# Performance work log

Measured on AMD Instinct MI355X. Metric: run time of the kernel, lower is better.

The kernel has to match this reference:

```python
import jax, jax.numpy as jnp
import numpy as np

B, L, DM, H, PD = 2, 1024, 512, 8, 64
D = DM // H  # head_dim = 64
NEG = -10000.0


def setup_inputs() -> dict:
    key = jax.random.key(0)
    ks = jax.random.split(key, 12)
    s = 1.0 / np.sqrt(DM)
    sp = 1.0 / np.sqrt(PD)
    return {
        "x": jax.random.normal(ks[0], (B, L, DM), dtype=jnp.float32),
        "z": jax.random.normal(ks[1], (B, L, L, PD), dtype=jnp.float32),
        "residue_mask": jnp.ones((B, L), dtype=bool),
        "Wq": jax.random.normal(ks[2], (DM, DM), dtype=jnp.float32) * s,
        "bq": jnp.zeros((DM,), dtype=jnp.float32),
        "Wk": jax.random.normal(ks[3], (DM, DM), dtype=jnp.float32) * s,
        "bk": jnp.zeros((DM,), dtype=jnp.float32),
        "Wv": jax.random.normal(ks[4], (DM, DM), dtype=jnp.float32) * s,
        "bv": jnp.zeros((DM,), dtype=jnp.float32),
        "Wo": jax.random.normal(ks[5], (DM, DM), dtype=jnp.float32) * s,
        "bo": jnp.zeros((DM,), dtype=jnp.float32),
        "Wpb": jax.random.normal(ks[6], (PD, H), dtype=jnp.float32) * sp,
    }


def reference(x, z, residue_mask, Wq, bq, Wk, bk, Wv, bv, Wo, bo, Wpb):
    b, l, c = x.shape
    scale = 1.0 / np.sqrt(D)
    # projections -> (B, H, L, D)
    q = (x @ Wq + bq).reshape(b, l, H, D).transpose(0, 2, 1, 3)
    k = (x @ Wk + bk).reshape(b, l, H, D).transpose(0, 2, 1, 3)
    v = (x @ Wv + bv).reshape(b, l, H, D).transpose(0, 2, 1, 3)
    # pair bias: (B, L, L, PD) @ (PD, H) -> (B, H, L, L)
    bias = jnp.einsum('bijp,ph->bhij', z, Wpb)
    logits = jnp.einsum('bhid,bhjd->bhij', q, k) * scale + bias
    key_ok = residue_mask[:, None, None, :]
    query_ok = residue_mask[:, None, :, None]
    logits = jnp.where(key_ok, logits, NEG)
    logits = jnp.where(query_ok, logits, NEG)
    attn = jax.nn.softmax(logits, axis=-1)
    out = jnp.einsum('bhij,bhjd->bhid', attn, v)
    out = out.transpose(0, 2, 1, 3).reshape(b, l, c)
    return out @ Wo + bo
```

## Files before the change

### kernel.cpp

```cpp
#include <hip/hip_runtime.h>

typedef __bf16 bf16;
typedef __attribute__((ext_vector_type(4))) __bf16 bf16x4;
typedef __attribute__((ext_vector_type(8))) __bf16 bf16x8;
typedef __attribute__((ext_vector_type(4))) float f32x4;
typedef __attribute__((ext_vector_type(4))) _Float16 f16x4;
typedef __attribute__((ext_vector_type(2))) _Float16 f16x2;

#define B_   2
#define L_   1024
#define DM_  512
#define H_   8
#define D_   64
#define PD_  64
#define NEG_VAL -10000.0f

static __device__ __forceinline__ f32x4 mfma_bf16(bf16x8 a, bf16x8 b, f32x4 c) {
  return __builtin_amdgcn_mfma_f32_16x16x32_bf16(a, b, c, 0, 0, 0);
}

__global__ __launch_bounds__(256) void prep_bias(
    const float* __restrict__ z, const float* __restrict__ Wpb, const int* __restrict__ mask,
    const float* __restrict__ x, const float* __restrict__ Wq, const float* __restrict__ Wk,
    const float* __restrict__ Wv, const float* __restrict__ Wo,
    _Float16* __restrict__ biasbuf, bf16* __restrict__ xb, bf16* __restrict__ Wt,
    bf16* __restrict__ Wto) {
  __shared__ char smem[18944];
  int bid = blockIdx.x, tid = threadIdx.x;
  if (bid < 2048) {
    _Float16 (*outt)[1032] = (_Float16(*)[1032])smem;
    float* wpb_lds = (float*)(smem + 16512);
    int w = tid >> 6, lane = tid & 63;
    int lr = lane & 15, lg = lane >> 4;
    int jc = bid & 15, it = (bid >> 4) & 63, b = bid >> 10;
    if (tid < 128) {
      f32x4 v = reinterpret_cast<const f32x4*>(Wpb)[tid];
      *reinterpret_cast<f32x4*>(wpb_lds + tid * 4) = v;
    }
    __syncthreads();
    bf16x8 wb0, wb1;
#pragma unroll
    for (int e = 0; e < 8; ++e) {
      wb0[e] = (lr < 8) ? (bf16)wpb_lds[(lg * 8 + e) * 8 + lr] : (bf16)0.0f;
      wb1[e] = (lr < 8) ? (bf16)wpb_lds[(lg * 8 + 32 + e) * 8 + lr] : (bf16)0.0f;
    }
#pragma unroll
    for (int ii = 0; ii < 4; ++ii) {
      int il = w * 4 + ii;
      int i = it * 16 + il;
#pragma unroll
      for (int js = 0; js < 4; ++js) {
        const float* zr = z + ((long)(b * L_ + i) * L_ + jc * 64 + js * 16 + lr) * 64 + lg * 8;
        f32x4 z0 = *reinterpret_cast<const f32x4*>(zr);
        f32x4 z1 = *reinterpret_cast<const f32x4*>(zr + 4);
        f32x4 z2 = *reinterpret_cast<const f32x4*>(zr + 32);
        f32x4 z3 = *reinterpret_cast<const f32x4*>(zr + 36);
        bf16x8 a0, a1;
#pragma unroll
        for (int e = 0; e < 4; ++e) {
          a0[e] = (bf16)z0[e]; a0[e + 4] = (bf16)z1[e];
          a1[e] = (bf16)z2[e]; a1[e + 4] = (bf16)z3[e];
        }
        f32x4 c = {0.f, 0.f, 0.f, 0.f};
        c = mfma_bf16(a0, wb0, c);
        c = mfma_bf16(a1, wb1, c);
        if (lr < 8) {
          int4 mk = *reinterpret_cast<const int4*>(mask + b * L_ + jc * 64 + js * 16 + lg * 4);
          f16x4 hv;
          hv[0] = mk.x ? (_Float16)c[0] : (_Float16)NEG_VAL;
          hv[1] = mk.y ? (_Float16)c[1] : (_Float16)NEG_VAL;
          hv[2] = mk.z ? (_Float16)c[2] : (_Float16)NEG_VAL;
          hv[3] = mk.w ? (_Float16)c[3] : (_Float16)NEG_VAL;
          *reinterpret_cast<f16x4*>(&outt[lr][((js * 4 + lg) * 16 + il) * 4]) = hv;
        }
      }
    }
    __syncthreads();
    {
      int h = tid & 7, part = tid >> 3;
      _Float16* dst = biasbuf + (((((long)b * H_ + h) * 64 + it) * 16 + jc) << 10) + part * 32;
      const _Float16* srcl = &outt[h][part * 32];
#pragma unroll
      for (int e = 0; e < 8; ++e)
        *reinterpret_cast<f16x4*>(dst + e * 4) = *reinterpret_cast<const f16x4*>(srcl + e * 4);
    }
  } else {
    int pbid = bid - 2048;
    if (pbid < 1024) {
      float (*td)[33] = (float(*)[33])smem;
      int r = tid >> 3, c4 = (tid & 7) * 4;
      const float* src;
      bf16* dstbase;
      int n0, k0, srcol;
      if (pbid < 768) {
        int nt2 = pbid >> 4, kt = pbid & 15;
        n0 = nt2 * 32; k0 = kt * 32;
        int sel = n0 >> 9;
        src = sel == 0 ? Wq : (sel == 1 ? Wk : Wv);
        srcol = n0 & 511;
        dstbase = Wt + (long)n0 * 512;
      } else {
        int t2 = pbid - 768;
        int nt2 = t2 >> 4, kt = t2 & 15;
        n0 = nt2 * 32; k0 = kt * 32;
        src = Wo; srcol = n0;
        dstbase = Wto + (long)n0 * 512;
      }
      f32x4 v = *reinterpret_cast<const f32x4*>(src + (long)(k0 + r) * 512 + srcol + c4);
#pragma unroll
      for (int e = 0; e < 4; ++e) td[r][c4 + e] = v[e];
      __syncthreads();
      int nl = tid >> 3, k4 = (tid & 7) * 4;
      bf16x4 o;
#pragma unroll
      for (int e = 0; e < 4; ++e) o[e] = (bf16)td[k4 + e][nl];
      *reinterpret_cast<bf16x4*>(dstbase + (long)nl * 512 + k0 + k4) = o;
    } else {
      int base = (pbid - 1024) * 1024 + tid * 4;
      f32x4 v = *reinterpret_cast<const f32x4*>(x + base);
      bf16x4 o;
#pragma unroll
      for (int e = 0; e < 4; ++e) o[e] = (bf16)v[e];
      *reinterpret_cast<bf16x4*>(xb + base) = o;
    }
  }
}

__global__ __launch_bounds__(256) void qkv_gemm(
    const bf16* __restrict__ xb, const bf16* __restrict__ Wt,
    const float* __restrict__ bq, const float* __restrict__ bk, const float* __restrict__ bv,
    bf16* __restrict__ qb, bf16* __restrict__ kb, bf16* __restrict__ vT) {
  __shared__ bf16 bpanel[16 * 520];
  int tid = threadIdx.x, w = tid >> 6, lane = tid & 63;
  int lr = lane & 15, lg = lane >> 4;
  int bid = blockIdx.x;
  int mt = bid / 96, nt = bid - mt * 96;
  int col0 = nt * 16;
  {
    const bf16* src = Wt + (long)col0 * 512;
#pragma unroll
    for (int q = 0; q < 4; ++q) {
      int off = q * 2048 + tid * 8;
      int row = off >> 9, col = off & 511;
      *reinterpret_cast<bf16x8*>(&bpanel[row * 520 + col]) =
          *reinterpret_cast<const bf16x8*>(src + off);
    }
  }
  __syncthreads();
  int m0base = mt * 128 + w * 32;
  const bf16* a0p = xb + (long)(m0base + lr) * 512 + lg * 8;
  const bf16* a1p = a0p + 16 * 512;
  f32x4 acc0 = {0.f, 0.f, 0.f, 0.f}, acc1 = acc0;
#pragma unroll
  for (int kk = 0; kk < 512; kk += 32) {
    bf16x8 a0 = *reinterpret_cast<const bf16x8*>(a0p + kk);
    bf16x8 a1 = *reinterpret_cast<const bf16x8*>(a1p + kk);
    bf16x8 b = *reinterpret_cast<const bf16x8*>(&bpanel[lr * 520 + kk + lg * 8]);
    acc0 = mfma_bf16(a0, b, acc0);
    acc1 = mfma_bf16(a1, b, acc1);
  }
  int col = col0 + lr;
  int wsel = col >> 9;
  int ncol = col & 511;
  int h = ncol >> 6, d = ncol & 63;
  const float* bias = wsel == 0 ? bq : (wsel == 1 ? bk : bv);
  float bval = bias[ncol];
#pragma unroll
  for (int mi = 0; mi < 2; ++mi) {
    f32x4 acc = (mi == 0) ? acc0 : acc1;
    int m0 = m0base + mi * 16 + lg * 4;
    int bidx = m0 >> 10, l0 = m0 & 1023;
    if (wsel == 2) {
      bf16x4 pv;
#pragma unroll
      for (int r = 0; r < 4; ++r) pv[r] = (bf16)(acc[r] + bval);
      *reinterpret_cast<bf16x4*>(vT + ((long)(bidx * H_ + h) * D_ + d) * L_ + l0) = pv;
    } else if (wsel == 0) {
#pragma unroll
      for (int r = 0; r < 4; ++r)
        qb[((long)(bidx * H_ + h) * L_ + l0 + r) * D_ + d] = (bf16)((acc[r] + bval) * 0.125f);
    } else {
#pragma unroll
      for (int r = 0; r < 4; ++r)
        kb[((long)(bidx * H_ + h) * L_ + l0 + r) * D_ + d] = (bf16)(acc[r] + bval);
    }
  }
}

__global__ __launch_bounds__(256) void attn_kernel(
    const bf16* __restrict__ qb, const bf16* __restrict__ kb, const bf16* __restrict__ vT,
    const _Float16* __restrict__ biasb, const int* __restrict__ mask, bf16* __restrict__ attn_out) {
  __shared__ bf16 p_lds[4][16 * 64];
  __shared__ float o_lds[4][16][68];
  __shared__ float m_lds[4][16];
  __shared__ float l_lds[4][16];
  int bid = blockIdx.x;
  int b = bid >> 9, h = (bid >> 6) & 7, it = bid & 63;
  int i0 = it * 16;
  int tid = threadIdx.x, w = tid >> 6, lane = tid & 63, lr = lane & 15, lg = lane >> 4;

  const bf16* qrow = qb + ((long)(b * H_ + h) * L_ + i0 + lr) * D_ + lg * 8;
  bf16x8 qa0 = *reinterpret_cast<const bf16x8*>(qrow);
  bf16x8 qa1 = *reinterpret_cast<const bf16x8*>(qrow + 32);
  const bf16* kbase = kb + (long)(b * H_ + h) * L_ * D_;
  const bf16* vbase = vT + (long)(b * H_ + h) * D_ * L_;
  const _Float16* bias_base = biasb + ((((long)(b * H_ + h) * 64 + it)) << 14);
  bool qok = mask[b * L_ + i0 + lr] != 0;

  float m = -3.0e38f, l = 0.f;
  f32x4 o0 = {0.f,0.f,0.f,0.f}, o1 = o0, o2 = o0, o3 = o0;
  char* pbuf = (char*)&p_lds[w][0];
  int swz = (lr & 7) << 4;

  for (int jt = 0; jt < 4; ++jt) {
    int j0 = w * 256 + jt * 64;
    const _Float16* btile = bias_base + ((w * 4 + jt) << 10);
    f32x4 s0, s1, s2, s3;
#pragma unroll
    for (int tile = 0; tile < 4; ++tile) {
      f16x4 bv = *reinterpret_cast<const f16x4*>(btile + ((tile * 4 + lg) * 16 + lr) * 4);
      f32x4 acc;
#pragma unroll
      for (int r = 0; r < 4; ++r) acc[r] = (float)bv[r];
      const bf16* kr = kbase + (long)(j0 + tile * 16 + lr) * D_ + lg * 8;
      acc = mfma_bf16(*reinterpret_cast<const bf16x8*>(kr), qa0, acc);
      acc = mfma_bf16(*reinterpret_cast<const bf16x8*>(kr + 32), qa1, acc);
      if (tile == 0) s0 = acc; else if (tile == 1) s1 = acc; else if (tile == 2) s2 = acc; else s3 = acc;
    }
    if (!qok) {
#pragma unroll
      for (int r = 0; r < 4; ++r) { s0[r] = NEG_VAL; s1[r] = NEG_VAL; s2[r] = NEG_VAL; s3[r] = NEG_VAL; }
    }
    float mt = s0[0];
#pragma unroll
    for (int r = 0; r < 4; ++r) mt = fmaxf(fmaxf(fmaxf(mt, s0[r]), fmaxf(s1[r], s2[r])), s3[r]);
    mt = fmaxf(mt, __shfl_xor(mt, 16));
    mt = fmaxf(mt, __shfl_xor(mt, 32));
    float mnew = fmaxf(m, mt);
    float alpha = __expf(m - mnew);
    m = mnew;
    f32x4 p0, p1, p2, p3;
    float ps = 0.f;
#pragma unroll
    for (int r = 0; r < 4; ++r) {
      p0[r] = __expf(s0[r] - mnew); p1[r] = __expf(s1[r] - mnew);
      p2[r] = __expf(s2[r] - mnew); p3[r] = __expf(s3[r] - mnew);
      ps += p0[r] + p1[r] + p2[r] + p3[r];
    }
    ps += __shfl_xor(ps, 16);
    ps += __shfl_xor(ps, 32);
    l = l * alpha + ps;
#pragma unroll
    for (int r = 0; r < 4; ++r) { o0[r] *= alpha; o1[r] *= alpha; o2[r] *= alpha; o3[r] *= alpha; }
#pragma unroll
    for (int tile = 0; tile < 4; ++tile) {
      f32x4 pv = (tile == 0) ? p0 : (tile == 1) ? p1 : (tile == 2) ? p2 : p3;
      bf16x4 pb_;
#pragma unroll
      for (int r = 0; r < 4; ++r) pb_[r] = (bf16)pv[r];
      *reinterpret_cast<bf16x4*>(pbuf + ((lr * 128 + tile * 32 + lg * 8) ^ swz)) = pb_;
    }
    bf16x8 pa0 = *reinterpret_cast<const bf16x8*>(pbuf + ((lr * 128 + lg * 16) ^ swz));
    bf16x8 pa1 = *reinterpret_cast<const bf16x8*>(pbuf + ((lr * 128 + 64 + lg * 16) ^ swz));
#pragma unroll
    for (int dtile = 0; dtile < 4; ++dtile) {
      const bf16* vr = vbase + (long)(dtile * 16 + lr) * L_ + j0 + lg * 8;
      f32x4 acc = (dtile == 0) ? o0 : (dtile == 1) ? o1 : (dtile == 2) ? o2 : o3;
      acc = mfma_bf16(*reinterpret_cast<const bf16x8*>(vr), pa0, acc);
      acc = mfma_bf16(*reinterpret_cast<const bf16x8*>(vr + 32), pa1, acc);
      if (dtile == 0) o0 = acc; else if (dtile == 1) o1 = acc; else if (dtile == 2) o2 = acc; else o3 = acc;
    }
  }
#pragma unroll
  for (int dtile = 0; dtile < 4; ++dtile) {
    f32x4 ov = (dtile == 0) ? o0 : (dtile == 1) ? o1 : (dtile == 2) ? o2 : o3;
    *reinterpret_cast<f32x4*>(&o_lds[w][lr][dtile * 16 + lg * 4]) = ov;
  }
  if (lg == 0) { m_lds[w][lr] = m; l_lds[w][lr] = l; }
  __syncthreads();
  {
    int row = tid >> 4, d0 = (tid & 15) * 4;
    float M = fmaxf(fmaxf(m_lds[0][row], m_lds[1][row]), fmaxf(m_lds[2][row], m_lds[3][row]));
    float lt = 0.f;
    float oacc[4] = {0.f, 0.f, 0.f, 0.f};
#pragma unroll
    for (int ww = 0; ww < 4; ++ww) {
      float c = __expf(m_lds[ww][row] - M);
      lt += c * l_lds[ww][row];
#pragma unroll
      for (int e = 0; e < 4; ++e) oacc[e] += c * o_lds[ww][row][d0 + e];
    }
    float inv = 1.0f / lt;
    bf16x4 ov;
#pragma unroll
    for (int e = 0; e < 4; ++e) ov[e] = (bf16)(oacc[e] * inv);
    *reinterpret_cast<bf16x4*>(attn_out + ((long)(b * L_ + i0 + row)) * DM_ + h * D_ + d0) = ov;
  }
}

__global__ __launch_bounds__(256) void out_gemm(
    const bf16* __restrict__ ab, const bf16* __restrict__ Wto,
    const float* __restrict__ bo, float* __restrict__ out) {
  int wid = blockIdx.x * 4 + (threadIdx.x >> 6);
  int lane = threadIdx.x & 63;
  int mt = wid >> 4, nt = wid & 15;
  int row0 = mt * 32, col0 = nt * 32;
  int lr = lane & 15, lg = lane >> 4;
  const bf16* a0p = ab + (row0 + lr) * 512 + lg * 8;
  const bf16* a1p = a0p + 16 * 512;
  const bf16* b0p = Wto + (col0 + lr) * 512 + lg * 8;
  const bf16* b1p = b0p + 16 * 512;
  f32x4 acc00 = {0.f,0.f,0.f,0.f}, acc01 = acc00, acc10 = acc00, acc11 = acc00;
#pragma unroll
  for (int kk = 0; kk < 512; kk += 32) {
    bf16x8 a0 = *reinterpret_cast<const bf16x8*>(a0p + kk);
    bf16x8 a1 = *reinterpret_cast<const bf16x8*>(a1p + kk);
    bf16x8 b0 = *reinterpret_cast<const bf16x8*>(b0p + kk);
    bf16x8 b1 = *reinterpret_cast<const bf16x8*>(b1p + kk);
    acc00 = mfma_bf16(a0, b0, acc00);
    acc01 = mfma_bf16(a0, b1, acc01);
    acc10 = mfma_bf16(a1, b0, acc10);
    acc11 = mfma_bf16(a1, b1, acc11);
  }
#pragma unroll
  for (int ni = 0; ni < 2; ++ni) {
    int col = col0 + ni * 16 + lr;
    float bval = bo[col];
#pragma unroll
    for (int mi = 0; mi < 2; ++mi) {
      f32x4 acc = (mi == 0) ? (ni == 0 ? acc00 : acc01) : (ni == 0 ? acc10 : acc11);
      int m0 = row0 + mi * 16 + lg * 4;
#pragma unroll
      for (int r = 0; r < 4; ++r) out[(long)(m0 + r) * 512 + col] = acc[r] + bval;
    }
  }
}

extern "C" void kernel_launch(void* const* d_in, const int* in_sizes, int n_in,
                              void* d_out, int out_size, void* d_ws, size_t ws_size,
                              hipStream_t stream) {
  const float* x    = (const float*)d_in[0];
  const float* z    = (const float*)d_in[1];
  const int*   mask = (const int*)d_in[2];
  const float* Wq   = (const float*)d_in[3];
  const float* bq   = (const float*)d_in[4];
  const float* Wk   = (const float*)d_in[5];
  const float* bk   = (const float*)d_in[6];
  const float* Wv   = (const float*)d_in[7];
  const float* bv   = (const float*)d_in[8];
  const float* Wo   = (const float*)d_in[9];
  const float* bo   = (const float*)d_in[10];
  const float* Wpb  = (const float*)d_in[11];

  char* ws = (char*)d_ws;
  bf16* xb        = (bf16*)(ws + 0);
  bf16* Wt        = (bf16*)(ws + 2097152);
  bf16* Wto       = (bf16*)(ws + 3670016);
  bf16* qbuf      = (bf16*)(ws + 4196352);
  bf16* kbuf      = (bf16*)(ws + 6293504);
  bf16* vTbuf     = (bf16*)(ws + 8390656);
  bf16* attn_out  = (bf16*)(ws + 10487808);
  _Float16* biasb = (_Float16*)(ws + 12584960);

  prep_bias<<<4096, 256, 0, stream>>>(z, Wpb, mask, x, Wq, Wk, Wv, Wo,
                                      biasb, xb, Wt, Wto);
  qkv_gemm<<<1536, 256, 0, stream>>>(xb, Wt, bq, bk, bv, qbuf, kbuf, vTbuf);
  attn_kernel<<<1024, 256, 0, stream>>>(qbuf, kbuf, vTbuf, biasb, mask, attn_out);
  out_gemm<<<256, 256, 0, stream>>>(attn_out, Wto, bo, (float*)d_out);
}
```

Baseline: 186.4 us.

## Fuse QKV projection into bias-prep kernel, converting fp32 inputs inline

Removes the separate QKV GEMM launch and the precomputed bf16 copies of x and the transposed Wq/Wk/Wv. The QKV GEMM blocks now run inside the front kernel alongside the pair-bias blocks. Each block reads fp32 x and W directly, transposes and converts W into LDS, and converts A fragments to bf16 in registers. This saves one launch and the intermediate workspace traffic, but every GEMM block reloads and reconverts fp32 data, with strided 2-byte LDS transposed stores that may bank-conflict.

```diff
diff --git a/kernel.cpp b/kernel.cpp
--- a/kernel.cpp
+++ b/kernel.cpp
@@ -5,7 +5,6 @@
 typedef __attribute__((ext_vector_type(8))) __bf16 bf16x8;
 typedef __attribute__((ext_vector_type(4))) float f32x4;
 typedef __attribute__((ext_vector_type(4))) _Float16 f16x4;
-typedef __attribute__((ext_vector_type(2))) _Float16 f16x2;
 
 #define B_   2
 #define L_   1024
@@ -19,12 +18,13 @@
   return __builtin_amdgcn_mfma_f32_16x16x32_bf16(a, b, c, 0, 0, 0);
 }
 
-__global__ __launch_bounds__(256) void prep_bias(
+__global__ __launch_bounds__(256) void front_kernel(
     const float* __restrict__ z, const float* __restrict__ Wpb, const int* __restrict__ mask,
     const float* __restrict__ x, const float* __restrict__ Wq, const float* __restrict__ Wk,
     const float* __restrict__ Wv, const float* __restrict__ Wo,
-    _Float16* __restrict__ biasbuf, bf16* __restrict__ xb, bf16* __restrict__ Wt,
-    bf16* __restrict__ Wto) {
+    const float* __restrict__ bq, const float* __restrict__ bk, const float* __restrict__ bv,
+    _Float16* __restrict__ biasbuf, bf16* __restrict__ Wto,
+    bf16* __restrict__ qb, bf16* __restrict__ kb, bf16* __restrict__ vT) {
   __shared__ char smem[18944];
   int bid = blockIdx.x, tid = threadIdx.x;
   if (bid < 2048) {
@@ -84,105 +84,84 @@
       for (int e = 0; e < 8; ++e)
         *reinterpret_cast<f16x4*>(dst + e * 4) = *reinterpret_cast<const f16x4*>(srcl + e * 4);
     }
+  } else if (bid < 2304) {
+    float (*td)[33] = (float(*)[33])smem;
+    int t2 = bid - 2048;
+    int nt2 = t2 >> 4, kt = t2 & 15;
+    int n0 = nt2 * 32, k0 = kt * 32;
+    int r = tid >> 3, c4 = (tid & 7) * 4;
+    f32x4 v = *reinterpret_cast<const f32x4*>(Wo + (long)(k0 + r) * 512 + n0 + c4);
+#pragma unroll
+    for (int e = 0; e < 4; ++e) td[r][c4 + e] = v[e];
+    __syncthreads();
+    int nl = tid >> 3, k4 = (tid & 7) * 4;
+    bf16x4 o;
+#pragma unroll
+    for (int e = 0; e < 4; ++e) o[e] = (bf16)td[k4 + e][nl];
+    *reinterpret_cast<bf16x4*>(Wto + (long)(n0 + nl) * 512 + k0 + k4) = o;
   } else {
-    int pbid = bid - 2048;
-    if (pbid < 1024) {
-      float (*td)[33] = (float(*)[33])smem;
-      int r = tid >> 3, c4 = (tid & 7) * 4;
-      const float* src;
-      bf16* dstbase;
-      int n0, k0, srcol;
-      if (pbid < 768) {
-        int nt2 = pbid >> 4, kt = pbid & 15;
-        n0 = nt2 * 32; k0 = kt * 32;
-        int sel = n0 >> 9;
-        src = sel == 0 ? Wq : (sel == 1 ? Wk : Wv);
-        srcol = n0 & 511;
-        dstbase = Wt + (long)n0 * 512;
+    bf16* bpanel = (bf16*)smem;
+    int pbid = bid - 2304;
+    int w = tid >> 6, lane = tid & 63;
+    int lr = lane & 15, lg = lane >> 4;
+    int mt = pbid / 96, nt = pbid - mt * 96;
+    int col0 = nt * 16;
+    int wsel = col0 >> 9;
+    int ncol0 = col0 & 511;
+    const float* wsrc = wsel == 0 ? Wq : (wsel == 1 ? Wk : Wv);
+#pragma unroll
+    for (int itr = 0; itr < 16; ++itr) {
+      int row = itr * 32 + (tid >> 3);
+      int cp = (tid & 7) * 2;
+      float2 v = *reinterpret_cast<const float2*>(wsrc + (long)row * 512 + ncol0 + cp);
+      bpanel[cp * 520 + row] = (bf16)v.x;
+      bpanel[(cp + 1) * 520 + row] = (bf16)v.y;
+    }
+    __syncthreads();
+    int m0base = mt * 128 + w * 32;
+    const float* a0f = x + (long)(m0base + lr) * 512;
+    const float* a1f = a0f + 16 * 512;
+    f32x4 acc0 = {0.f, 0.f, 0.f, 0.f}, acc1 = acc0;
+#pragma unroll
+    for (int kk = 0; kk < 512; kk += 32) {
+      f32x4 a0lo = *reinterpret_cast<const f32x4*>(a0f + kk + lg * 8);
+      f32x4 a0hi = *reinterpret_cast<const f32x4*>(a0f + kk + lg * 8 + 4);
+      f32x4 a1lo = *reinterpret_cast<const f32x4*>(a1f + kk + lg * 8);
+      f32x4 a1hi = *reinterpret_cast<const f32x4*>(a1f + kk + lg * 8 + 4);
+      bf16x8 a0, a1;
+#pragma unroll
+      for (int e = 0; e < 4; ++e) {
+        a0[e] = (bf16)a0lo[e]; a0[e + 4] = (bf16)a0hi[e];
+        a1[e] = (bf16)a1lo[e]; a1[e + 4] = (bf16)a1hi[e];
+      }
+      bf16x8 bfrag = *reinterpret_cast<const bf16x8*>(&bpanel[lr * 520 + kk + lg * 8]);
+      acc0 = mfma_bf16(a0, bfrag, acc0);
+      acc1 = mfma_bf16(a1, bfrag, acc1);
+    }
+    int col = col0 + lr;
+    int ncol = col & 511;
+    int h = ncol >> 6, d = ncol & 63;
+    const float* bias = wsel == 0 ? bq : (wsel == 1 ? bk : bv);
+    float bval = bias[ncol];
+#pragma unroll
+    for (int mi = 0; mi < 2; ++mi) {
+      f32x4 acc = (mi == 0) ? acc0 : acc1;
+      int m0 = m0base + mi * 16 + lg * 4;
+      int bidx = m0 >> 10, l0 = m0 & 1023;
+      if (wsel == 2) {
+        bf16x4 pv;
+#pragma unroll
+        for (int r = 0; r < 4; ++r) pv[r] = (bf16)(acc[r] + bval);
+        *reinterpret_cast<bf16x4*>(vT + ((long)(bidx * H_ + h) * D_ + d) * L_ + l0) = pv;
+      } else if (wsel == 0) {
+#pragma unroll
+        for (int r = 0; r < 4; ++r)
+          qb[((long)(bidx * H_ + h) * L_ + l0 + r) * D_ + d] = (bf16)((acc[r] + bval) * 0.125f);
       } else {
-        int t2 = pbid - 768;
-        int nt2 = t2 >> 4, kt = t2 & 15;
-        n0 = nt2 * 32; k0 = kt * 32;
-        src = Wo; srcol = n0;
-        dstbase = Wto + (long)n0 * 512;
+#pragma unroll
+        for (int r = 0; r < 4; ++r)
+          kb[((long)(bidx * H_ + h) * L_ + l0 + r) * D_ + d] = (bf16)(acc[r] + bval);
       }
-      f32x4 v = *reinterpret_cast<const f32x4*>(src + (long)(k0 + r) * 512 + srcol + c4);
-#pragma unroll
-      for (int e = 0; e < 4; ++e) td[r][c4 + e] = v[e];
-      __syncthreads();
-      int nl = tid >> 3, k4 = (tid & 7) * 4;
-      bf16x4 o;
-#pragma unroll
-      for (int e = 0; e < 4; ++e) o[e] = (bf16)td[k4 + e][nl];
-      *reinterpret_cast<bf16x4*>(dstbase + (long)nl * 512 + k0 + k4) = o;
-    } else {
-      int base = (pbid - 1024) * 1024 + tid * 4;
-      f32x4 v = *reinterpret_cast<const f32x4*>(x + base);
-      bf16x4 o;
-#pragma unroll
-      for (int e = 0; e < 4; ++e) o[e] = (bf16)v[e];
-      *reinterpret_cast<bf16x4*>(xb + base) = o;
-    }
-  }
-}
-
-__global__ __launch_bounds__(256) void qkv_gemm(
-    const bf16* __restrict__ xb, const bf16* __restrict__ Wt,
-    const float* __restrict__ bq, const float* __restrict__ bk, const float* __restrict__ bv,
-    bf16* __restrict__ qb, bf16* __restrict__ kb, bf16* __restrict__ vT) {
-  __shared__ bf16 bpanel[16 * 520];
-  int tid = threadIdx.x, w = tid >> 6, lane = tid & 63;
-  int lr = lane & 15, lg = lane >> 4;
-  int bid = blockIdx.x;
-  int mt = bid / 96, nt = bid - mt * 96;
-  int col0 = nt * 16;
-  {
-    const bf16* src = Wt + (long)col0 * 512;
-#pragma unroll
-    for (int q = 0; q < 4; ++q) {
-      int off = q * 2048 + tid * 8;
-      int row = off >> 9, col = off & 511;
-      *reinterpret_cast<bf16x8*>(&bpanel[row * 520 + col]) =
-          *reinterpret_cast<const bf16x8*>(src + off);
-    }
-  }
-  __syncthreads();
-  int m0base = mt * 128 + w * 32;
-  const bf16* a0p = xb + (long)(m0base + lr) * 512 + lg * 8;
-  const bf16* a1p = a0p + 16 * 512;
-  f32x4 acc0 = {0.f, 0.f, 0.f, 0.f}, acc1 = acc0;
-#pragma unroll
-  for (int kk = 0; kk < 512; kk += 32) {
-    bf16x8 a0 = *reinterpret_cast<const bf16x8*>(a0p + kk);
-    bf16x8 a1 = *reinterpret_cast<const bf16x8*>(a1p + kk);
-    bf16x8 b = *reinterpret_cast<const bf16x8*>(&bpanel[lr * 520 + kk + lg * 8]);
-    acc0 = mfma_bf16(a0, b, acc0);
-    acc1 = mfma_bf16(a1, b, acc1);
-  }
-  int col = col0 + lr;
-  int wsel = col >> 9;
-  int ncol = col & 511;
-  int h = ncol >> 6, d = ncol & 63;
-  const float* bias = wsel == 0 ? bq : (wsel == 1 ? bk : bv);
-  float bval = bias[ncol];
-#pragma unroll
-  for (int mi = 0; mi < 2; ++mi) {
-    f32x4 acc = (mi == 0) ? acc0 : acc1;
-    int m0 = m0base + mi * 16 + lg * 4;
-    int bidx = m0 >> 10, l0 = m0 & 1023;
-    if (wsel == 2) {
-      bf16x4 pv;
-#pragma unroll
-      for (int r = 0; r < 4; ++r) pv[r] = (bf16)(acc[r] + bval);
-      *reinterpret_cast<bf16x4*>(vT + ((long)(bidx * H_ + h) * D_ + d) * L_ + l0) = pv;
-    } else if (wsel == 0) {
-#pragma unroll
-      for (int r = 0; r < 4; ++r)
-        qb[((long)(bidx * H_ + h) * L_ + l0 + r) * D_ + d] = (bf16)((acc[r] + bval) * 0.125f);
-    } else {
-#pragma unroll
-      for (int r = 0; r < 4; ++r)
-        kb[((long)(bidx * H_ + h) * L_ + l0 + r) * D_ + d] = (bf16)(acc[r] + bval);
     }
   }
 }
@@ -353,18 +332,15 @@
   const float* Wpb  = (const float*)d_in[11];
 
   char* ws = (char*)d_ws;
-  bf16* xb        = (bf16*)(ws + 0);
-  bf16* Wt        = (bf16*)(ws + 2097152);
-  bf16* Wto       = (bf16*)(ws + 3670016);
-  bf16* qbuf      = (bf16*)(ws + 4196352);
-  bf16* kbuf      = (bf16*)(ws + 6293504);
-  bf16* vTbuf     = (bf16*)(ws + 8390656);
-  bf16* attn_out  = (bf16*)(ws + 10487808);
-  _Float16* biasb = (_Float16*)(ws + 12584960);
-
-  prep_bias<<<4096, 256, 0, stream>>>(z, Wpb, mask, x, Wq, Wk, Wv, Wo,
-                                      biasb, xb, Wt, Wto);
-  qkv_gemm<<<1536, 256, 0, stream>>>(xb, Wt, bq, bk, bv, qbuf, kbuf, vTbuf);
+  bf16* Wto       = (bf16*)(ws + 0);
+  bf16* qbuf      = (bf16*)(ws + 524288);
+  bf16* kbuf      = (bf16*)(ws + 2621440);
+  bf16* vTbuf     = (bf16*)(ws + 4718592);
+  bf16* attn_out  = (bf16*)(ws + 6815744);
+  _Float16* biasb = (_Float16*)(ws + 8912896);
+
+  front_kernel<<<3840, 256, 0, stream>>>(z, Wpb, mask, x, Wq, Wk, Wv, Wo,
+                                         bq, bk, bv, biasb, Wto, qbuf, kbuf, vTbuf);
   attn_kernel<<<1024, 256, 0, stream>>>(qbuf, kbuf, vTbuf, biasb, mask, attn_out);
   out_gemm<<<256, 256, 0, stream>>>(attn_out, Wto, bo, (float*)d_out);
 }
```

After: 200.2 us. +7.4%, slower.

## Stage z tiles through swizzled LDS with fine-grained blocks and row-major bias layout

Applied to the files above, without the earlier changes.

The pair-bias prep kernel now uses many small blocks, each loading a contiguous 16KB chunk of z with coalesced vector loads into an XOR-swizzled LDS buffer, instead of strided per-lane global reads. The bias buffer layout changes from tiled to plain row-major (b,h,i,j), and the attention kernel's bias load addressing is updated to match. The aim is better coalescing of the dominant z read. The cost is a much larger grid with more per-block overhead and syncs, narrow f16x2 output stores, and strided bias reads in attention.

```diff
diff --git a/kernel.cpp b/kernel.cpp
--- a/kernel.cpp
+++ b/kernel.cpp
@@ -25,18 +25,27 @@
     const float* __restrict__ Wv, const float* __restrict__ Wo,
     _Float16* __restrict__ biasbuf, bf16* __restrict__ xb, bf16* __restrict__ Wt,
     bf16* __restrict__ Wto) {
-  __shared__ char smem[18944];
+  __shared__ char smem[19584];
   int bid = blockIdx.x, tid = threadIdx.x;
-  if (bid < 2048) {
-    _Float16 (*outt)[1032] = (_Float16(*)[1032])smem;
-    float* wpb_lds = (float*)(smem + 16512);
+  if (bid < 32768) {
+    float* zt_raw = (float*)smem;
+    _Float16 (*bt)[72] = (_Float16(*)[72])(smem + 16384);
+    float* wpb_lds = (float*)(smem + 17536);
     int w = tid >> 6, lane = tid & 63;
     int lr = lane & 15, lg = lane >> 4;
-    int jc = bid & 15, it = (bid >> 4) & 63, b = bid >> 10;
     if (tid < 128) {
       f32x4 v = reinterpret_cast<const f32x4*>(Wpb)[tid];
       *reinterpret_cast<f32x4*>(wpb_lds + tid * 4) = v;
     }
+    char* zb = (char*)zt_raw;
+    const char* zsrc = (const char*)(z + (long)bid * 4096);
+#pragma unroll
+    for (int q = 0; q < 4; ++q) {
+      int lb = q * 4096 + tid * 16;
+      int row = lb >> 8, col = lb & 255;
+      f32x4 v = *reinterpret_cast<const f32x4*>(zsrc + lb);
+      *reinterpret_cast<f32x4*>(zb + row * 256 + (col ^ ((row & 7) << 5))) = v;
+    }
     __syncthreads();
     bf16x8 wb0, wb1;
 #pragma unroll
@@ -44,48 +53,42 @@
       wb0[e] = (lr < 8) ? (bf16)wpb_lds[(lg * 8 + e) * 8 + lr] : (bf16)0.0f;
       wb1[e] = (lr < 8) ? (bf16)wpb_lds[(lg * 8 + 32 + e) * 8 + lr] : (bf16)0.0f;
     }
-#pragma unroll
-    for (int ii = 0; ii < 4; ++ii) {
-      int il = w * 4 + ii;
-      int i = it * 16 + il;
-#pragma unroll
-      for (int js = 0; js < 4; ++js) {
-        const float* zr = z + ((long)(b * L_ + i) * L_ + jc * 64 + js * 16 + lr) * 64 + lg * 8;
-        f32x4 z0 = *reinterpret_cast<const f32x4*>(zr);
-        f32x4 z1 = *reinterpret_cast<const f32x4*>(zr + 4);
-        f32x4 z2 = *reinterpret_cast<const f32x4*>(zr + 32);
-        f32x4 z3 = *reinterpret_cast<const f32x4*>(zr + 36);
-        bf16x8 a0, a1;
-#pragma unroll
-        for (int e = 0; e < 4; ++e) {
-          a0[e] = (bf16)z0[e]; a0[e + 4] = (bf16)z1[e];
-          a1[e] = (bf16)z2[e]; a1[e + 4] = (bf16)z3[e];
-        }
-        f32x4 c = {0.f, 0.f, 0.f, 0.f};
-        c = mfma_bf16(a0, wb0, c);
-        c = mfma_bf16(a1, wb1, c);
-        if (lr < 8) {
-          int4 mk = *reinterpret_cast<const int4*>(mask + b * L_ + jc * 64 + js * 16 + lg * 4);
-          f16x4 hv;
-          hv[0] = mk.x ? (_Float16)c[0] : (_Float16)NEG_VAL;
-          hv[1] = mk.y ? (_Float16)c[1] : (_Float16)NEG_VAL;
-          hv[2] = mk.z ? (_Float16)c[2] : (_Float16)NEG_VAL;
-          hv[3] = mk.w ? (_Float16)c[3] : (_Float16)NEG_VAL;
-          *reinterpret_cast<f16x4*>(&outt[lr][((js * 4 + lg) * 16 + il) * 4]) = hv;
-        }
-      }
+    int row = w * 16 + lr;
+    int sw = (row & 7) << 5;
+    const char* zr = zb + row * 256;
+    f32x4 z0 = *reinterpret_cast<const f32x4*>(zr + ((lg * 32) ^ sw));
+    f32x4 z1 = *reinterpret_cast<const f32x4*>(zr + (((lg * 32) ^ sw) + 16));
+    f32x4 z2 = *reinterpret_cast<const f32x4*>(zr + ((128 + lg * 32) ^ sw));
+    f32x4 z3 = *reinterpret_cast<const f32x4*>(zr + (((128 + lg * 32) ^ sw) + 16));
+    bf16x8 a0, a1;
+#pragma unroll
+    for (int e = 0; e < 4; ++e) { a0[e] = (bf16)z0[e]; a0[e + 4] = (bf16)z1[e]; }
+#pragma unroll
+    for (int e = 0; e < 4; ++e) { a1[e] = (bf16)z2[e]; a1[e + 4] = (bf16)z3[e]; }
+    f32x4 acc = {0.f, 0.f, 0.f, 0.f};
+    acc = mfma_bf16(a0, wb0, acc);
+    acc = mfma_bf16(a1, wb1, acc);
+    __syncthreads();
+    if (lr < 8) {
+      f16x4 hv;
+#pragma unroll
+      for (int r = 0; r < 4; ++r) hv[r] = (_Float16)acc[r];
+      *reinterpret_cast<f16x4*>(&bt[lr][w * 16 + lg * 4]) = hv;
     }
     __syncthreads();
     {
-      int h = tid & 7, part = tid >> 3;
-      _Float16* dst = biasbuf + (((((long)b * H_ + h) * 64 + it) * 16 + jc) << 10) + part * 32;
-      const _Float16* srcl = &outt[h][part * 32];
-#pragma unroll
-      for (int e = 0; e < 8; ++e)
-        *reinterpret_cast<f16x4*>(dst + e * 4) = *reinterpret_cast<const f16x4*>(srcl + e * 4);
+      int h = tid >> 5, part = tid & 31;
+      long pb = (long)bid * 64;
+      int b = (int)(pb >> 20), i = ((int)(pb >> 10)) & 1023, j0 = (int)pb & 1023;
+      int j = j0 + part * 2;
+      f16x2 v = *reinterpret_cast<const f16x2*>(&bt[h][part * 2]);
+      if (mask[b * L_ + j] == 0)     v[0] = (_Float16)NEG_VAL;
+      if (mask[b * L_ + j + 1] == 0) v[1] = (_Float16)NEG_VAL;
+      _Float16* dst = biasbuf + ((((long)b * H_ + h) * L_ + i) << 10) + j;
+      *reinterpret_cast<f16x2*>(dst) = v;
     }
   } else {
-    int pbid = bid - 2048;
+    int pbid = bid - 32768;
     if (pbid < 1024) {
       float (*td)[33] = (float(*)[33])smem;
       int r = tid >> 3, c4 = (tid & 7) * 4;
@@ -204,7 +207,7 @@
   bf16x8 qa1 = *reinterpret_cast<const bf16x8*>(qrow + 32);
   const bf16* kbase = kb + (long)(b * H_ + h) * L_ * D_;
   const bf16* vbase = vT + (long)(b * H_ + h) * D_ * L_;
-  const _Float16* bias_base = biasb + ((((long)(b * H_ + h) * 64 + it)) << 14);
+  const _Float16* bias_base = biasb + ((long)(b * H_ + h) * L_ + i0) * L_;
   bool qok = mask[b * L_ + i0 + lr] != 0;
 
   float m = -3.0e38f, l = 0.f;
@@ -214,11 +217,10 @@
 
   for (int jt = 0; jt < 4; ++jt) {
     int j0 = w * 256 + jt * 64;
-    const _Float16* btile = bias_base + ((w * 4 + jt) << 10);
     f32x4 s0, s1, s2, s3;
 #pragma unroll
     for (int tile = 0; tile < 4; ++tile) {
-      f16x4 bv = *reinterpret_cast<const f16x4*>(btile + ((tile * 4 + lg) * 16 + lr) * 4);
+      f16x4 bv = *reinterpret_cast<const f16x4*>(bias_base + (long)lr * L_ + j0 + tile * 16 + lg * 4);
       f32x4 acc;
 #pragma unroll
       for (int r = 0; r < 4; ++r) acc[r] = (float)bv[r];
@@ -362,8 +364,8 @@
   bf16* attn_out  = (bf16*)(ws + 10487808);
   _Float16* biasb = (_Float16*)(ws + 12584960);
 
-  prep_bias<<<4096, 256, 0, stream>>>(z, Wpb, mask, x, Wq, Wk, Wv, Wo,
-                                      biasb, xb, Wt, Wto);
+  prep_bias<<<34816, 256, 0, stream>>>(z, Wpb, mask, x, Wq, Wk, Wv, Wo,
+                                       biasb, xb, Wt, Wto);
   qkv_gemm<<<1536, 256, 0, stream>>>(xb, Wt, bq, bk, bv, qbuf, kbuf, vTbuf);
   attn_kernel<<<1024, 256, 0, stream>>>(qbuf, kbuf, vTbuf, biasb, mask, attn_out);
   out_gemm<<<256, 256, 0, stream>>>(attn_out, Wto, bo, (float*)d_out);
```

Measured after the change: 175.3 us. 5.9% less time.
